# Kernel optimization log

Hardware: AMD Instinct MI355X
Metric: run time of the kernel (lower is better)

The kernel has to match this reference:

```python
import jax, jax.numpy as jnp
import numpy as np

HEADS = 16
KV_HEADS = 4
DIM_HEAD = 64
DIM = 1024
B, N = 2, 2048


def setup_inputs() -> dict:
    key = jax.random.key(0)
    k1, k2, k3 = jax.random.split(key, 3)
    x = jax.random.normal(k1, (B, N, DIM), dtype=jnp.float32)
    Wq = jax.random.normal(k2, (DIM, HEADS * DIM_HEAD), dtype=jnp.float32) / np.sqrt(DIM)
    Wkv = jax.random.normal(k3, (DIM, 2 * KV_HEADS * DIM_HEAD), dtype=jnp.float32) / np.sqrt(DIM)
    k_scale = jnp.ones((HEADS, 1, DIM_HEAD), dtype=jnp.float32)
    return {"x": x, "Wq": Wq, "Wkv": Wkv, "k_scale": k_scale}


def reference(x, Wq, Wkv, k_scale):
    b, n, _ = x.shape
    g = HEADS // KV_HEADS  # query heads per kv head
    scale = DIM_HEAD ** -0.5
    # fused qkv projections (no bias)
    q = (x @ Wq).reshape(b, n, HEADS, DIM_HEAD)
    kv = x @ Wkv
    k, v = jnp.split(kv, 2, axis=-1)
    k = k.reshape(b, n, KV_HEADS, DIM_HEAD).transpose(0, 2, 1, 3)  # b k n d
    v = v.reshape(b, n, KV_HEADS, DIM_HEAD).transpose(0, 2, 1, 3)  # b k n d
    # group query heads: b, kv_heads, g, n, d
    qg = q.transpose(0, 2, 1, 3).reshape(b, KV_HEADS, g, n, DIM_HEAD)
    # per-query-head k scale, applied to the group-broadcast k (qk-norm)
    ks = k_scale.reshape(KV_HEADS, g, 1, DIM_HEAD)
    kk = k[:, :, None, :, :] * ks  # b k g n d
    dots = jnp.einsum('bkgid,bkgjd->bkgij', qg, kk) * scale
    attn = jax.nn.softmax(dots, axis=-1)
    out = jnp.einsum('bkgij,bkjd->bkgid', attn, v)  # v broadcast over g
    out = out.reshape(b, HEADS, n, DIM_HEAD).transpose(0, 2, 1, 3).reshape(b, n, HEADS * DIM_HEAD)
    return out
```

## Files before the change

kernel.cpp:

```cpp
#include <hip/hip_runtime.h>
#include <stdint.h>
#include <math.h>

typedef __attribute__((ext_vector_type(8))) __bf16 bf16x8;
typedef __attribute__((ext_vector_type(4))) float f32x4;
typedef __attribute__((ext_vector_type(16))) float f32x16;

__device__ __forceinline__ uint32_t f32_to_bf16_rne(float f) {
  union { float f; uint32_t u; } v; v.f = f;
  return (v.u + 0x7FFFu + ((v.u >> 16) & 1u)) >> 16;
}

__device__ __forceinline__ uint32_t cvt_pk_bf16(float lo, float hi) {
  uint32_t r;
  asm("v_cvt_pk_bf16_f32 %0, %1, %2" : "=v"(r) : "v"(lo), "v"(hi));
  return r;
}

__device__ __forceinline__ void gld16(void* lds, const void* g) {
  __builtin_amdgcn_global_load_lds(
      (__attribute__((address_space(1))) void*)(g),
      (__attribute__((address_space(3))) void*)(lds), 16, 0, 0);
}

__device__ __forceinline__ f32x4 mfma16(bf16x8 a, bf16x8 b, f32x4 c) {
  return __builtin_amdgcn_mfma_f32_16x16x32_bf16(a, b, c, 0, 0, 0);
}
__device__ __forceinline__ f32x16 mfma32(bf16x8 a, bf16x8 b, f32x16 c) {
  return __builtin_amdgcn_mfma_f32_32x32x16_bf16(a, b, c, 0, 0, 0);
}

#define LOG2E 1.44269504088896340736f

__global__ __launch_bounds__(256) void k_convert_x(const float* __restrict__ x,
                                                   uint16_t* __restrict__ xb) {
  int i = blockIdx.x * 256 + threadIdx.x;
  const float4* xv = (const float4*)x;
  float4 a = xv[2 * i], b2 = xv[2 * i + 1];
  uint32_t w0 = f32_to_bf16_rne(a.x) | (f32_to_bf16_rne(a.y) << 16);
  uint32_t w1 = f32_to_bf16_rne(a.z) | (f32_to_bf16_rne(a.w) << 16);
  uint32_t w2 = f32_to_bf16_rne(b2.x) | (f32_to_bf16_rne(b2.y) << 16);
  uint32_t w3 = f32_to_bf16_rne(b2.z) | (f32_to_bf16_rne(b2.w) << 16);
  ((uint4*)xb)[i] = make_uint4(w0, w1, w2, w3);
}

__global__ __launch_bounds__(256) void k_convert_w(const float* __restrict__ wq,
                                                   const float* __restrict__ wkv,
                                                   uint16_t* __restrict__ wt) {
  __shared__ float tile[64][65];
  int c0 = blockIdx.x * 64, k0 = blockIdx.y * 64;
  int t = threadIdx.x;
  int col = t & 63, rq = t >> 6;
#pragma unroll
  for (int rr = 0; rr < 16; rr++) {
    int r = rr * 4 + rq;
    int c = c0 + col;
    float v = (c < 1024) ? wq[(uint64_t)(k0 + r) * 1024 + c]
                         : wkv[(uint64_t)(k0 + r) * 512 + (c - 1024)];
    tile[r][col] = v;
  }
  __syncthreads();
#pragma unroll
  for (int rr = 0; rr < 16; rr++) {
    int a = rr * 4 + rq;
    wt[(uint64_t)(c0 + a) * 1024 + k0 + col] = (uint16_t)f32_to_bf16_rne(tile[col][a]);
  }
}

__global__ __launch_bounds__(256, 3) void k_proj_gemm(
    const uint16_t* __restrict__ xb, const uint16_t* __restrict__ wt,
    const float* __restrict__ kscale, uint16_t* __restrict__ q_ws,
    uint16_t* __restrict__ kf_ws, uint16_t* __restrict__ vf_ws) {
  __shared__ __align__(16) uint16_t ring[3][6144];
  int t = threadIdx.x;
  int w = t >> 6, l = t & 63;
  int lq = l & 15, lg = l >> 4;
  int m0 = blockIdx.x * 128, n0 = blockIdx.y * 64;
  int wr = w >> 1, wc = w & 1;
  f32x4 acc[4][2] = {};

  auto stage = [&](int slot, int k0) {
#pragma unroll
    for (int j = 0; j < 2; j++) {
      int tt = j * 256 + t;
      int r = tt >> 2, s = tt & 3;
      int sl = s ^ ((r >> 1) & 3);
      gld16((char*)&ring[slot][0] + (j * 256 + w * 64) * 16,
            xb + (uint64_t)(m0 + r) * 1024 + k0 + sl * 8);
    }
    {
      int r = t >> 2, s = t & 3;
      int sl = s ^ ((r >> 1) & 3);
      gld16((char*)&ring[slot][4096] + (w * 64) * 16,
            wt + (uint64_t)(n0 + r) * 1024 + k0 + sl * 8);
    }
  };

  stage(0, 0);
  stage(1, 32);
  asm volatile("s_waitcnt vmcnt(3)" ::: "memory");
  __builtin_amdgcn_s_barrier();

  for (int it = 0; it < 32; ++it) {
    int k0 = it * 32;
    int kn = k0 + 64;
    if (kn > 992) kn = 992;
    stage((it + 2) % 3, kn);

    const uint16_t* As = &ring[it % 3][0];
    const uint16_t* Bs = &ring[it % 3][4096];
    bf16x8 af[4], bfr[2];
#pragma unroll
    for (int m = 0; m < 4; m++) {
      int r = wr * 64 + m * 16 + lq;
      int s = lg ^ ((r >> 1) & 3);
      af[m] = *(const bf16x8*)(As + r * 32 + s * 8);
    }
#pragma unroll
    for (int n = 0; n < 2; n++) {
      int r = wc * 32 + n * 16 + lq;
      int s = lg ^ ((r >> 1) & 3);
      bfr[n] = *(const bf16x8*)(Bs + r * 32 + s * 8);
    }
    __builtin_amdgcn_s_setprio(1);
#pragma unroll
    for (int m = 0; m < 4; m++)
#pragma unroll
      for (int n = 0; n < 2; n++)
        acc[m][n] = mfma16(af[m], bfr[n], acc[m][n]);
    __builtin_amdgcn_s_setprio(0);
    asm volatile("s_waitcnt vmcnt(3) lgkmcnt(0)" ::: "memory");
    __builtin_amdgcn_s_barrier();
  }

#pragma unroll
  for (int m = 0; m < 4; m++)
#pragma unroll
    for (int n = 0; n < 2; n++)
#pragma unroll
      for (int jj = 0; jj < 4; jj++) {
        int row = m0 + wr * 64 + m * 16 + 4 * lg + jj;
        int col = n0 + wc * 32 + n * 16 + lq;
        float val = acc[m][n][jj];
        int b = row >> 11, nn = row & 2047;
        if (col < 1024) {
          val *= kscale[col] * 0.125f * LOG2E;
          q_ws[((uint64_t)((b * 16 + (col >> 6)) * 2048 + nn)) * 64 + (col & 63)] =
              (uint16_t)f32_to_bf16_rne(val);
        } else if (col < 1280) {
          int kvh = (col - 1024) >> 6;
          int d = col & 63;
          int gsu = nn >> 5, lrr = nn & 31;
          int mm = d >> 4, hh = (d >> 3) & 1, el = d & 7;
          kf_ws[(uint64_t)(b * 4 + kvh) * 131072 +
                (uint64_t)((((gsu * 4 + mm) * 64) + hh * 32 + lrr) * 8 + el)] =
              (uint16_t)f32_to_bf16_rne(val);
        } else {
          int kvh = (col - 1280) >> 6;
          int d = col & 63;
          int gsu = nn >> 5, jj2 = (nn >> 4) & 1, hh = (nn >> 3) & 1, el = nn & 7;
          int dd = d >> 5, lrr = d & 31;
          vf_ws[(uint64_t)(b * 4 + kvh) * 131072 +
                (uint64_t)((((gsu * 4 + dd * 2 + jj2) * 64) + hh * 32 + lrr) * 8 + el)] =
              (uint16_t)f32_to_bf16_rne(val);
        }
      }
}

__global__ __launch_bounds__(512, 4) void k_attn(const uint16_t* __restrict__ q_ws,
                                                 const uint16_t* __restrict__ kf_ws,
                                                 const uint16_t* __restrict__ vf_ws,
                                                 float* __restrict__ out) {
  __shared__ __align__(16) char smem[65536];

  int t = threadIdx.x, w = t >> 6, l = t & 63;
  int lr = l & 31, hi = l >> 5;
  int wq = w & 3, half = w >> 2;
  int blk = blockIdx.x;
  int c = blk & 7, j = blk >> 3;
  int b = c >> 2, kvh = c & 3;
  int h = kvh * 4 + (j >> 4), qb = j & 15;

  const uint16_t* Qb = q_ws + (uint64_t)(b * 16 + h) * 2048 * 64;
  const uint16_t* Kb = kf_ws + (uint64_t)(b * 4 + kvh) * 131072;
  const uint16_t* Vb = vf_ws + (uint64_t)(b * 4 + kvh) * 131072;
  int qrow0 = qb * 128 + wq * 32;

  bf16x8 qfrag[4];
#pragma unroll
  for (int m = 0; m < 4; m++)
    qfrag[m] = *(const bf16x8*)(Qb + (uint64_t)(qrow0 + lr) * 64 + m * 16 + hi * 8);

  f32x16 oacc[2] = {};
  float l_run = 0.f;

  const uint16_t* Sb = (wq < 2) ? Kb : Vb;
  auto stage = [&](int slot, int sul) {
    int gsu = half * 32 + sul;
    char* dst = smem + slot * 16384 + half * 8192 + wq * 2048 + l * 16;
    const uint16_t* src = Sb + (uint64_t)(gsu * 4 + (wq & 1) * 2) * 512 + l * 8;
    gld16(dst, src);
    gld16(dst + 1024, src + 512);
  };

  stage(0, 0);
  stage(1, 1);
  stage(2, 2);
  asm volatile("s_waitcnt vmcnt(4)" ::: "memory");
  __builtin_amdgcn_s_barrier();

  for (int su = 0; su < 32; ++su) {
    int sn = su + 3;
    if (sn > 31) sn = 31;
    stage((su + 3) & 3, sn);

    const uint16_t* base = (const uint16_t*)(smem + (su & 3) * 16384 + half * 8192);
    bf16x8 kf[4], vf[4];
#pragma unroll
    for (int m = 0; m < 4; m++) kf[m] = *(const bf16x8*)(base + m * 512 + l * 8);
#pragma unroll
    for (int i = 0; i < 4; i++) vf[i] = *(const bf16x8*)(base + (4 + i) * 512 + l * 8);

    f32x16 Tacc = {};
    __builtin_amdgcn_s_setprio(1);
#pragma unroll
    for (int m = 0; m < 4; m++) Tacc = mfma32(kf[m], qfrag[m], Tacc);
    __builtin_amdgcn_s_setprio(0);

    float p[16];
#pragma unroll
    for (int e = 0; e < 16; e++) p[e] = __builtin_amdgcn_exp2f(Tacc[e]);
    float sm0 = ((p[0] + p[1]) + (p[2] + p[3])) + ((p[4] + p[5]) + (p[6] + p[7]));
    float sm1 = ((p[8] + p[9]) + (p[10] + p[11])) + ((p[12] + p[13]) + (p[14] + p[15]));
    l_run += sm0 + sm1;

    bf16x8 pa[2];
#pragma unroll
    for (int jj = 0; jj < 2; jj++) {
      const float* pp = p + 8 * jj;
      uint32_t X = cvt_pk_bf16(pp[0], pp[1]);
      uint32_t Z = cvt_pk_bf16(pp[2], pp[3]);
      uint32_t Y = cvt_pk_bf16(pp[4], pp[5]);
      uint32_t W2 = cvt_pk_bf16(pp[6], pp[7]);
      asm volatile("v_permlane32_swap_b32 %0, %1" : "+v"(X), "+v"(Y));
      asm volatile("v_permlane32_swap_b32 %0, %1" : "+v"(Z), "+v"(W2));
      union { uint32_t u[4]; bf16x8 v; } pu;
      pu.u[0] = X; pu.u[1] = Z; pu.u[2] = Y; pu.u[3] = W2;
      pa[jj] = pu.v;
    }

    __builtin_amdgcn_s_setprio(1);
#pragma unroll
    for (int dd = 0; dd < 2; dd++)
#pragma unroll
      for (int jj = 0; jj < 2; jj++)
        oacc[dd] = mfma32(pa[jj], vf[dd * 2 + jj], oacc[dd]);
    __builtin_amdgcn_s_setprio(0);

    asm volatile("s_waitcnt vmcnt(4) lgkmcnt(0)" ::: "memory");
    __builtin_amdgcn_s_barrier();
  }

  l_run += __shfl_xor(l_run, 32);

  asm volatile("s_waitcnt vmcnt(0)" ::: "memory");
  __syncthreads();

  float* exch = (float*)smem;
  float* exl = (float*)(smem + 32768);
  if (half == 1) {
#pragma unroll
    for (int r = 0; r < 16; r++) {
      int qr = (r & 3) + 8 * (r >> 2) + 4 * hi;
      exch[wq * 2048 + qr * 64 + lr] = oacc[0][r];
      exch[wq * 2048 + qr * 64 + 32 + lr] = oacc[1][r];
    }
    if (hi == 0) exl[wq * 32 + lr] = l_run;
  }
  __syncthreads();
  if (half == 0) {
    l_run += exl[wq * 32 + lr];
    float inv = 1.0f / l_run;
#pragma unroll
    for (int r = 0; r < 16; r++) {
      int qr = (r & 3) + 8 * (r >> 2) + 4 * hi;
      float iv = __shfl(inv, qr);
      float o0 = oacc[0][r] + exch[wq * 2048 + qr * 64 + lr];
      float o1 = oacc[1][r] + exch[wq * 2048 + qr * 64 + 32 + lr];
      float* orow = out + (uint64_t)(b * 2048 + qrow0 + qr) * 1024 + h * 64 + lr;
      orow[0] = o0 * iv;
      orow[32] = o1 * iv;
    }
  }
}

extern "C" void kernel_launch(void* const* d_in, const int* in_sizes, int n_in,
                              void* d_out, int out_size, void* d_ws, size_t ws_size,
                              hipStream_t stream) {
  const float* x = (const float*)d_in[0];
  const float* wq = (const float*)d_in[1];
  const float* wkv = (const float*)d_in[2];
  const float* kscale = (const float*)d_in[3];
  float* out = (float*)d_out;
  char* ws = (char*)d_ws;
  uint16_t* xb = (uint16_t*)(ws);
  uint16_t* wt = (uint16_t*)(ws + (8ull << 20));
  uint16_t* q_ws = (uint16_t*)(ws + (11ull << 20));
  uint16_t* kf_ws = (uint16_t*)(ws + (19ull << 20));
  uint16_t* vf_ws = (uint16_t*)(ws + (21ull << 20));

  k_convert_x<<<2048, 256, 0, stream>>>(x, xb);
  k_convert_w<<<dim3(24, 16), 256, 0, stream>>>(wq, wkv, wt);
  k_proj_gemm<<<dim3(32, 24), 256, 0, stream>>>(xb, wt, kscale, q_ws, kf_ws, vf_ws);
  k_attn<<<512, 512, 0, stream>>>(q_ws, kf_ws, vf_ws, out);
}
```

Before: 80.47 us.

## Merge convert kernels and software-pipeline GEMM and attention main loops

Merges the x and weight bf16 conversion kernels into one launch, saving a kernel launch and the gap between launches. The projection GEMM moves from a 3-slot to a 4-slot LDS ring and double-buffers register fragments, so LDS reads for the next step overlap the current MFMAs. The attention loop is software-pipelined: the QK^T MFMAs for the next key block are issued before the exp/PV of the current block, and the vmcnt wait is relaxed. This raises LDS use and register pressure and could lower occupancy.

```diff
diff --git a/kernel.cpp b/kernel.cpp
--- a/kernel.cpp
+++ b/kernel.cpp
@@ -32,38 +32,41 @@
 
 #define LOG2E 1.44269504088896340736f
 
-__global__ __launch_bounds__(256) void k_convert_x(const float* __restrict__ x,
-                                                   uint16_t* __restrict__ xb) {
-  int i = blockIdx.x * 256 + threadIdx.x;
-  const float4* xv = (const float4*)x;
-  float4 a = xv[2 * i], b2 = xv[2 * i + 1];
-  uint32_t w0 = f32_to_bf16_rne(a.x) | (f32_to_bf16_rne(a.y) << 16);
-  uint32_t w1 = f32_to_bf16_rne(a.z) | (f32_to_bf16_rne(a.w) << 16);
-  uint32_t w2 = f32_to_bf16_rne(b2.x) | (f32_to_bf16_rne(b2.y) << 16);
-  uint32_t w3 = f32_to_bf16_rne(b2.z) | (f32_to_bf16_rne(b2.w) << 16);
-  ((uint4*)xb)[i] = make_uint4(w0, w1, w2, w3);
-}
-
-__global__ __launch_bounds__(256) void k_convert_w(const float* __restrict__ wq,
-                                                   const float* __restrict__ wkv,
-                                                   uint16_t* __restrict__ wt) {
+__global__ __launch_bounds__(256) void k_convert(const float* __restrict__ x,
+                                                 const float* __restrict__ wq,
+                                                 const float* __restrict__ wkv,
+                                                 uint16_t* __restrict__ xb,
+                                                 uint16_t* __restrict__ wt) {
   __shared__ float tile[64][65];
-  int c0 = blockIdx.x * 64, k0 = blockIdx.y * 64;
+  int blk = blockIdx.x;
   int t = threadIdx.x;
-  int col = t & 63, rq = t >> 6;
-#pragma unroll
-  for (int rr = 0; rr < 16; rr++) {
-    int r = rr * 4 + rq;
-    int c = c0 + col;
-    float v = (c < 1024) ? wq[(uint64_t)(k0 + r) * 1024 + c]
-                         : wkv[(uint64_t)(k0 + r) * 512 + (c - 1024)];
-    tile[r][col] = v;
-  }
-  __syncthreads();
-#pragma unroll
-  for (int rr = 0; rr < 16; rr++) {
-    int a = rr * 4 + rq;
-    wt[(uint64_t)(c0 + a) * 1024 + k0 + col] = (uint16_t)f32_to_bf16_rne(tile[col][a]);
+  if (blk < 2048) {
+    int i = blk * 256 + t;
+    const float4* xv = (const float4*)x;
+    float4 a = xv[2 * i], b2 = xv[2 * i + 1];
+    uint32_t w0 = f32_to_bf16_rne(a.x) | (f32_to_bf16_rne(a.y) << 16);
+    uint32_t w1 = f32_to_bf16_rne(a.z) | (f32_to_bf16_rne(a.w) << 16);
+    uint32_t w2 = f32_to_bf16_rne(b2.x) | (f32_to_bf16_rne(b2.y) << 16);
+    uint32_t w3 = f32_to_bf16_rne(b2.z) | (f32_to_bf16_rne(b2.w) << 16);
+    ((uint4*)xb)[i] = make_uint4(w0, w1, w2, w3);
+  } else {
+    int blk2 = blk - 2048;
+    int c0 = (blk2 % 24) * 64, k0 = (blk2 / 24) * 64;
+    int col = t & 63, rq = t >> 6;
+#pragma unroll
+    for (int rr = 0; rr < 16; rr++) {
+      int r = rr * 4 + rq;
+      int c = c0 + col;
+      float v = (c < 1024) ? wq[(uint64_t)(k0 + r) * 1024 + c]
+                           : wkv[(uint64_t)(k0 + r) * 512 + (c - 1024)];
+      tile[r][col] = v;
+    }
+    __syncthreads();
+#pragma unroll
+    for (int rr = 0; rr < 16; rr++) {
+      int a = rr * 4 + rq;
+      wt[(uint64_t)(c0 + a) * 1024 + k0 + col] = (uint16_t)f32_to_bf16_rne(tile[col][a]);
+    }
   }
 }
 
@@ -71,7 +74,7 @@
     const uint16_t* __restrict__ xb, const uint16_t* __restrict__ wt,
     const float* __restrict__ kscale, uint16_t* __restrict__ q_ws,
     uint16_t* __restrict__ kf_ws, uint16_t* __restrict__ vf_ws) {
-  __shared__ __align__(16) uint16_t ring[3][6144];
+  __shared__ __align__(16) uint16_t ring[4][6144];
   int t = threadIdx.x;
   int w = t >> 6, l = t & 63;
   int lq = l & 15, lg = l >> 4;
@@ -96,41 +99,52 @@
     }
   };
 
-  stage(0, 0);
-  stage(1, 32);
-  asm volatile("s_waitcnt vmcnt(3)" ::: "memory");
-  __builtin_amdgcn_s_barrier();
-
-  for (int it = 0; it < 32; ++it) {
-    int k0 = it * 32;
-    int kn = k0 + 64;
-    if (kn > 992) kn = 992;
-    stage((it + 2) % 3, kn);
-
-    const uint16_t* As = &ring[it % 3][0];
-    const uint16_t* Bs = &ring[it % 3][4096];
-    bf16x8 af[4], bfr[2];
+  struct PFrags { bf16x8 a[4]; bf16x8 b[2]; };
+  auto readFrags = [&](PFrags& F, int slot) {
+    const uint16_t* As = &ring[slot][0];
+    const uint16_t* Bs = &ring[slot][4096];
 #pragma unroll
     for (int m = 0; m < 4; m++) {
       int r = wr * 64 + m * 16 + lq;
       int s = lg ^ ((r >> 1) & 3);
-      af[m] = *(const bf16x8*)(As + r * 32 + s * 8);
+      F.a[m] = *(const bf16x8*)(As + r * 32 + s * 8);
     }
 #pragma unroll
     for (int n = 0; n < 2; n++) {
       int r = wc * 32 + n * 16 + lq;
       int s = lg ^ ((r >> 1) & 3);
-      bfr[n] = *(const bf16x8*)(Bs + r * 32 + s * 8);
-    }
+      F.b[n] = *(const bf16x8*)(Bs + r * 32 + s * 8);
+    }
+  };
+
+  auto pbody = [&](int tt2, PFrags& C, PFrags& N) {
+    int kn = (tt2 + 3) * 32;
+    if (kn > 992) kn = 992;
+    stage((tt2 + 3) & 3, kn);
     __builtin_amdgcn_s_setprio(1);
 #pragma unroll
     for (int m = 0; m < 4; m++)
 #pragma unroll
       for (int n = 0; n < 2; n++)
-        acc[m][n] = mfma16(af[m], bfr[n], acc[m][n]);
+        acc[m][n] = mfma16(C.a[m], C.b[n], acc[m][n]);
     __builtin_amdgcn_s_setprio(0);
+    int tn = tt2 + 1;
+    if (tn > 31) tn = 31;
+    readFrags(N, tn & 3);
     asm volatile("s_waitcnt vmcnt(3) lgkmcnt(0)" ::: "memory");
     __builtin_amdgcn_s_barrier();
+  };
+
+  stage(0, 0);
+  stage(1, 32);
+  stage(2, 64);
+  asm volatile("s_waitcnt vmcnt(3)" ::: "memory");
+  __builtin_amdgcn_s_barrier();
+  PFrags FA, FB;
+  readFrags(FA, 0);
+  for (int sp = 0; sp < 16; ++sp) {
+    pbody(2 * sp, FA, FB);
+    pbody(2 * sp + 1, FB, FA);
   }
 
 #pragma unroll
@@ -203,33 +217,14 @@
     gld16(dst + 1024, src + 512);
   };
 
-  stage(0, 0);
-  stage(1, 1);
-  stage(2, 2);
-  asm volatile("s_waitcnt vmcnt(4)" ::: "memory");
-  __builtin_amdgcn_s_barrier();
-
-  for (int su = 0; su < 32; ++su) {
-    int sn = su + 3;
-    if (sn > 31) sn = 31;
-    stage((su + 3) & 3, sn);
-
-    const uint16_t* base = (const uint16_t*)(smem + (su & 3) * 16384 + half * 8192);
-    bf16x8 kf[4], vf[4];
-#pragma unroll
-    for (int m = 0; m < 4; m++) kf[m] = *(const bf16x8*)(base + m * 512 + l * 8);
-#pragma unroll
-    for (int i = 0; i < 4; i++) vf[i] = *(const bf16x8*)(base + (4 + i) * 512 + l * 8);
-
-    f32x16 Tacc = {};
-    __builtin_amdgcn_s_setprio(1);
-#pragma unroll
-    for (int m = 0; m < 4; m++) Tacc = mfma32(kf[m], qfrag[m], Tacc);
-    __builtin_amdgcn_s_setprio(0);
-
+  auto slotbase = [&](int slot) {
+    return (const uint16_t*)(smem + slot * 16384 + half * 8192);
+  };
+
+  auto finish = [&](f32x16& Tc, const uint16_t* baseC) {
     float p[16];
 #pragma unroll
-    for (int e = 0; e < 16; e++) p[e] = __builtin_amdgcn_exp2f(Tacc[e]);
+    for (int e = 0; e < 16; e++) p[e] = __builtin_amdgcn_exp2f(Tc[e]);
     float sm0 = ((p[0] + p[1]) + (p[2] + p[3])) + ((p[4] + p[5]) + (p[6] + p[7]));
     float sm1 = ((p[8] + p[9]) + (p[10] + p[11])) + ((p[12] + p[13]) + (p[14] + p[15]));
     l_run += sm0 + sm1;
@@ -249,6 +244,9 @@
       pa[jj] = pu.v;
     }
 
+    bf16x8 vf[4];
+#pragma unroll
+    for (int i = 0; i < 4; i++) vf[i] = *(const bf16x8*)(baseC + (4 + i) * 512 + l * 8);
     __builtin_amdgcn_s_setprio(1);
 #pragma unroll
     for (int dd = 0; dd < 2; dd++)
@@ -256,10 +254,47 @@
       for (int jj = 0; jj < 2; jj++)
         oacc[dd] = mfma32(pa[jj], vf[dd * 2 + jj], oacc[dd]);
     __builtin_amdgcn_s_setprio(0);
-
-    asm volatile("s_waitcnt vmcnt(4) lgkmcnt(0)" ::: "memory");
+  };
+
+  auto body = [&](int su, f32x16& Tc, f32x16& Tn) {
+    int sn = su + 3;
+    if (sn > 31) sn = 31;
+    stage((su + 3) & 3, sn);
+    const uint16_t* baseN = slotbase((su + 1) & 3);
+    bf16x8 kf[4];
+#pragma unroll
+    for (int m = 0; m < 4; m++) kf[m] = *(const bf16x8*)(baseN + m * 512 + l * 8);
+    Tn = (f32x16){};
+    __builtin_amdgcn_s_setprio(1);
+#pragma unroll
+    for (int m = 0; m < 4; m++) Tn = mfma32(kf[m], qfrag[m], Tn);
+    __builtin_amdgcn_s_setprio(0);
+    finish(Tc, slotbase(su & 3));
+    asm volatile("s_waitcnt vmcnt(2) lgkmcnt(0)" ::: "memory");
     __builtin_amdgcn_s_barrier();
-  }
+  };
+
+  stage(0, 0);
+  stage(1, 1);
+  stage(2, 2);
+  asm volatile("s_waitcnt vmcnt(2)" ::: "memory");
+  __builtin_amdgcn_s_barrier();
+
+  f32x16 TA = {}, TB = {};
+  {
+    const uint16_t* b0 = slotbase(0);
+    bf16x8 kf0[4];
+#pragma unroll
+    for (int m = 0; m < 4; m++) kf0[m] = *(const bf16x8*)(b0 + m * 512 + l * 8);
+#pragma unroll
+    for (int m = 0; m < 4; m++) TA = mfma32(kf0[m], qfrag[m], TA);
+  }
+  for (int sp = 0; sp < 15; ++sp) {
+    body(2 * sp, TA, TB);
+    body(2 * sp + 1, TB, TA);
+  }
+  body(30, TA, TB);
+  finish(TB, slotbase(3));
 
   l_run += __shfl_xor(l_run, 32);
 
@@ -309,8 +344,7 @@
   uint16_t* kf_ws = (uint16_t*)(ws + (19ull << 20));
   uint16_t* vf_ws = (uint16_t*)(ws + (21ull << 20));
 
-  k_convert_x<<<2048, 256, 0, stream>>>(x, xb);
-  k_convert_w<<<dim3(24, 16), 256, 0, stream>>>(wq, wkv, wt);
+  k_convert<<<2432, 256, 0, stream>>>(x, wq, wkv, xb, wt);
   k_proj_gemm<<<dim3(32, 24), 256, 0, stream>>>(xb, wt, kscale, q_ws, kf_ws, vf_ws);
   k_attn<<<512, 512, 0, stream>>>(q_ws, kf_ws, vf_ws, out);
 }
```

Result: no change. 78.94 us (-1.9%).
